# Optimization experiments

Measured on AMD Instinct MI355X. Metric: run time of the kernel, lower is better.

Reference implementation:

```python
import jax, jax.numpy as jnp
import numpy as np

BN_EPS = 1e-5


def setup_inputs() -> dict:
    key = jax.random.key(0)
    ks = jax.random.split(key, 6)
    B, N, M, C1, C2 = 8, 8192, 2048, 128, 256
    in_ch = C1 + C2  # 384
    return {
        "xyz1": jax.random.uniform(ks[0], (B, N, 3), dtype=jnp.float32),
        "xyz2": jax.random.uniform(ks[1], (B, M, 3), dtype=jnp.float32),
        "features1": jax.random.normal(ks[2], (B, C1, N), dtype=jnp.float32),
        "features2": jax.random.normal(ks[3], (B, C2, M), dtype=jnp.float32),
        # Conv1d(kernel_size=1, bias=False) weights, squeezed to [out, in]
        "conv_w0": jax.random.normal(ks[4], (256, in_ch), dtype=jnp.float32) * 0.05,
        "gamma0": jnp.ones((256,), dtype=jnp.float32),
        "beta0": jnp.zeros((256,), dtype=jnp.float32),
        "conv_w1": jax.random.normal(ks[5], (256, 256), dtype=jnp.float32) * 0.05,
        "gamma1": jnp.ones((256,), dtype=jnp.float32),
        "beta1": jnp.zeros((256,), dtype=jnp.float32),
    }


def _conv_bn_relu(x, w, gamma, beta):
    # 1x1 Conv1d (no bias) == per-point channel matmul: [B,Cin,N] -> [B,Cout,N]
    x = jnp.einsum("oc,bcn->bon", w, x)
    # BatchNorm1d in training mode: batch stats over (B, N), biased variance
    mu = jnp.mean(x, axis=(0, 2), keepdims=True)
    var = jnp.var(x, axis=(0, 2), keepdims=True)
    x = (x - mu) * jax.lax.rsqrt(var + BN_EPS)
    x = x * gamma[None, :, None] + beta[None, :, None]
    return jax.nn.relu(x)


def reference(xyz1, xyz2, features1, features2,
              conv_w0, gamma0, beta0, conv_w1, gamma1, beta1):
    # squared pairwise distances [B, N, M] (broadcast diff reduced over coord dim)
    diff = xyz1[:, :, None, :] - xyz2[:, None, :, :]  # [B,N,M,3]
    dists = jnp.sum(diff * diff, axis=-1)             # [B,N,M]
    idx = jnp.argmin(dists, axis=-1)                  # [B,N] nearest downsampled point

    # per-batch gather: features2[b, :, idx[b]] -> [B, C2, N]
    interp = jax.vmap(lambda f, i: f[:, i])(features2, idx)

    x = jnp.concatenate([features1, interp], axis=1)  # [B, C1+C2, N]
    x = _conv_bn_relu(x, conv_w0, gamma0, beta0)
    x = _conv_bn_relu(x, conv_w1, gamma1, beta1)
    return x
```

## Files before the change

### kernel.cpp

```cpp
#include <hip/hip_runtime.h>
#include <stdint.h>

typedef unsigned short u16;
typedef unsigned int u32;
typedef __attribute__((ext_vector_type(8))) short short8;
typedef __attribute__((ext_vector_type(4))) float floatx4;

__device__ __forceinline__ u16 f2b(float f) {
  union { float f; u32 u; } c; c.f = f;
  u32 u = c.u;
  u += 0x7fffu + ((u >> 16) & 1u);
  return (u16)(u >> 16);
}
__device__ __forceinline__ float b2f(u16 h) {
  union { u32 u; float f; } c; c.u = ((u32)h) << 16;
  return c.f;
}

__device__ __forceinline__ void glds16(const void* g, void* l) {
  __builtin_amdgcn_global_load_lds((__attribute__((address_space(1))) void*)g,
                                   (__attribute__((address_space(3))) void*)l, 16, 0, 0);
}

__global__ void prep_all_k(const float* __restrict__ xyz1, const float* __restrict__ xyz2,
                           float2* __restrict__ cand,
                           const float* __restrict__ f1, u16* __restrict__ f1t,
                           const float* __restrict__ f2, u16* __restrict__ f2t,
                           const float* __restrict__ w0, u16* __restrict__ w0b,
                           const float* __restrict__ w1, u16* __restrict__ w1b,
                           float* __restrict__ sums) {
  __shared__ __align__(16) char smem[9216];
  int blk = blockIdx.x, t = threadIdx.x;
  if (blk < 512) {
    float4* s2 = (float4*)smem;
    int nq = blk & 7, mq = (blk >> 3) & 7, b = blk >> 6;
    const float* x2 = xyz2 + ((size_t)b * 2048 + mq * 256) * 3;
    s2[t] = make_float4(x2[t * 3], x2[t * 3 + 1], x2[t * 3 + 2], 0.f);
    __syncthreads();
    int n0 = nq * 1024 + t;
    float px[4], py[4], pz[4];
#pragma unroll
    for (int q = 0; q < 4; q++) {
      const float* p1 = xyz1 + ((size_t)b * 8192 + n0 + q * 256) * 3;
      px[q] = p1[0]; py[q] = p1[1]; pz[q] = p1[2];
    }
    float best[4] = {3.0e38f, 3.0e38f, 3.0e38f, 3.0e38f};
    int bi[4] = {0, 0, 0, 0};
#pragma unroll 4
    for (int m = 0; m < 256; m++) {
      float4 qq = s2[m];
#pragma unroll
      for (int q = 0; q < 4; q++) {
        float dx = px[q] - qq.x, dy = py[q] - qq.y, dz = pz[q] - qq.z;
        float d = fmaf(dz, dz, fmaf(dy, dy, dx * dx));
        bool c = d < best[q];
        best[q] = c ? d : best[q];
        bi[q] = c ? m : bi[q];
      }
    }
#pragma unroll
    for (int q = 0; q < 4; q++) {
      int n = n0 + q * 256;
      cand[(size_t)mq * 65536 + (size_t)b * 8192 + n] =
          make_float2(best[q], __int_as_float(mq * 256 + bi[q]));
    }
  } else if (blk < 3584) {
    const float* in; u16* out; int C, N, bx, by, bz;
    if (blk < 2560) { int rel = blk - 512;  in = f1; out = f1t; C = 128; N = 8192; bx = rel & 127; by = (rel >> 7) & 1; bz = rel >> 8; }
    else            { int rel = blk - 2560; in = f2; out = f2t; C = 256; N = 2048; bx = rel & 31;  by = (rel >> 5) & 3; bz = rel >> 7; }
    u16 (*tile)[72] = (u16(*)[72])smem;
    int c0 = by * 64, n0 = bx * 64;
    const float* src = in + ((size_t)bz * C + c0) * N + n0;
#pragma unroll
    for (int i = 0; i < 4; i++) {
      int id = t + i * 256;
      int c = id >> 4, nq = (id & 15) * 4;
      float4 v = *(const float4*)(src + (size_t)c * N + nq);
      tile[nq + 0][c] = f2b(v.x);
      tile[nq + 1][c] = f2b(v.y);
      tile[nq + 2][c] = f2b(v.z);
      tile[nq + 3][c] = f2b(v.w);
    }
    __syncthreads();
    int n = t >> 2, ch = (t & 3) * 16;
    u16* dst = out + ((size_t)bz * N + n0 + n) * C + c0 + ch;
    *(uint4*)dst = *(const uint4*)&tile[n][ch];
    *(uint4*)(dst + 8) = *(const uint4*)&tile[n][ch + 8];
  } else {
    int rel = blk - 3584;
    int i = rel * 256 + t;
    if (rel < 384) w0b[i] = f2b(w0[i]);
    else { int j = i - 98304; w1b[j] = f2b(w1[j]); }
    if (rel < 4) sums[i] = 0.f;
  }
}

__global__ __launch_bounds__(512) void gemm1_k(const u16* __restrict__ w0b, const u16* __restrict__ f1t,
                                               const u16* __restrict__ f2t, const float2* __restrict__ cand,
                                               float* __restrict__ sum0, float* __restrict__ sq0,
                                               u16* __restrict__ y0) {
  __shared__ u16 As[256 * 64];
  __shared__ u16 Bs[128 * 64];
  __shared__ int sidx[128];
  int t = threadIdx.x;
  int pt0 = blockIdx.x * 128;
  int b = pt0 >> 13;
  if (t < 128) {
    int p = pt0 + t;
    float bd = 3.0e38f; int bi = 0;
#pragma unroll
    for (int qc = 0; qc < 8; qc++) {
      float2 c = cand[(size_t)qc * 65536 + p];
      if (c.x < bd) { bd = c.x; bi = __float_as_int(c.y); }
    }
    sidx[t] = bi;
  }
  floatx4 zero = {0.f, 0.f, 0.f, 0.f};
  floatx4 acc[4][4];
#pragma unroll
  for (int i = 0; i < 4; i++)
#pragma unroll
    for (int j = 0; j < 4; j++) acc[i][j] = zero;
  int lane = t & 63, wave = t >> 6;
  int wrow = (wave >> 1) * 64, wcol = (wave & 1) * 64;
  int lr = lane & 15, lq = lane >> 4;
  int srow = lane >> 3;
  int sch = ((lane & 7) ^ srow) * 8;
  __syncthreads();
  int prow[2], gidx[2];
#pragma unroll
  for (int i = 0; i < 2; i++) {
    prow[i] = (wave * 2 + i) * 8 + srow;
    gidx[i] = sidx[prow[i]];
  }

#pragma unroll
  for (int k0 = 0; k0 < 384; k0 += 64) {
    __syncthreads();
#pragma unroll
    for (int i = 0; i < 4; i++) {
      int chunkA = wave * 4 + i;
      glds16(w0b + (size_t)(chunkA * 8 + srow) * 384 + k0 + sch, &As[chunkA * 512]);
    }
    if (k0 < 128) {
#pragma unroll
      for (int i = 0; i < 2; i++)
        glds16(f1t + (size_t)(pt0 + prow[i]) * 128 + k0 + sch, &Bs[(wave * 2 + i) * 512]);
    } else {
#pragma unroll
      for (int i = 0; i < 2; i++)
        glds16(f2t + ((size_t)(b << 11) + gidx[i]) * 256 + (k0 - 128) + sch, &Bs[(wave * 2 + i) * 512]);
    }
    __syncthreads();
#pragma unroll
    for (int ks = 0; ks < 2; ks++) {
      short8 af[4], bf[4];
#pragma unroll
      for (int i = 0; i < 4; i++) {
        int row = wrow + i * 16 + lr;
        af[i] = *(const short8*)&As[row * 64 + ((((ks << 2) | lq) ^ (lr & 7)) << 3)];
      }
#pragma unroll
      for (int j = 0; j < 4; j++) {
        int row = wcol + j * 16 + lr;
        bf[j] = *(const short8*)&Bs[row * 64 + ((((ks << 2) | lq) ^ (lr & 7)) << 3)];
      }
#pragma unroll
      for (int i = 0; i < 4; i++)
#pragma unroll
        for (int j = 0; j < 4; j++)
          acc[i][j] = __builtin_amdgcn_mfma_f32_16x16x32_bf16(af[i], bf[j], acc[i][j], 0, 0, 0);
    }
  }
#pragma unroll
  for (int i = 0; i < 4; i++) {
#pragma unroll
    for (int j = 0; j < 4; j++) {
      int o = wrow + i * 16 + lq * 4;
      int p = pt0 + wcol + j * 16 + lr;
      uint2 pk;
      pk.x = (u32)f2b(acc[i][j][0]) | ((u32)f2b(acc[i][j][1]) << 16);
      pk.y = (u32)f2b(acc[i][j][2]) | ((u32)f2b(acc[i][j][3]) << 16);
      *(uint2*)&y0[(size_t)p * 256 + o] = pk;
    }
  }
  __syncthreads();
  float* red = (float*)As;
  red[t] = 0.f;
  __syncthreads();
#pragma unroll
  for (int i = 0; i < 4; i++) {
#pragma unroll
    for (int r = 0; r < 4; r++) {
      float s = acc[i][0][r] + acc[i][1][r] + acc[i][2][r] + acc[i][3][r];
      float q = acc[i][0][r] * acc[i][0][r] + acc[i][1][r] * acc[i][1][r] +
                acc[i][2][r] * acc[i][2][r] + acc[i][3][r] * acc[i][3][r];
#pragma unroll
      for (int m = 8; m >= 1; m >>= 1) { s += __shfl_xor(s, m); q += __shfl_xor(q, m); }
      if (lr == 0) {
        int o = wrow + i * 16 + lq * 4 + r;
        atomicAdd(&red[o], s);
        atomicAdd(&red[256 + o], q);
      }
    }
  }
  __syncthreads();
  if (t < 256) {
    atomicAdd(&sum0[t], red[t]);
    atomicAdd(&sq0[t], red[256 + t]);
  }
}

__global__ __launch_bounds__(512) void gemm2_k(const u16* __restrict__ w1b, const u16* __restrict__ y0,
                                               const float* __restrict__ sum0, const float* __restrict__ sq0,
                                               const float* __restrict__ gamma0, const float* __restrict__ beta0,
                                               float* __restrict__ sum1, float* __restrict__ sq1,
                                               u16* __restrict__ y1) {
  __shared__ u16 As[256 * 64];
  __shared__ u16 Bs[128 * 72];
  __shared__ float ssc[256], ssh[256];
  int t = threadIdx.x;
  if (t < 256) {
    float mean = sum0[t] * (1.f / 65536.f);
    float var = fmaxf(sq0[t] * (1.f / 65536.f) - mean * mean, 0.f);
    float r = rsqrtf(var + 1e-5f);
    float sc = gamma0[t] * r;
    ssc[t] = sc;
    ssh[t] = beta0[t] - mean * sc;
  }
  int pt0 = blockIdx.x * 128;
  floatx4 zero = {0.f, 0.f, 0.f, 0.f};
  floatx4 acc[4][4];
#pragma unroll
  for (int i = 0; i < 4; i++)
#pragma unroll
    for (int j = 0; j < 4; j++) acc[i][j] = zero;
  int lane = t & 63, wave = t >> 6;
  int wrow = (wave >> 1) * 64, wcol = (wave & 1) * 64;
  int lr = lane & 15, lq = lane >> 4;
  int srow = lane >> 3;
  int sch = ((lane & 7) ^ srow) * 8;

#pragma unroll
  for (int k0 = 0; k0 < 256; k0 += 64) {
    __syncthreads();
#pragma unroll
    for (int i = 0; i < 4; i++) {
      int chunkA = wave * 4 + i;
      glds16(w1b + (size_t)(chunkA * 8 + srow) * 256 + k0 + sch, &As[chunkA * 512]);
    }
#pragma unroll
    for (int i = 0; i < 2; i++) {
      int id = t + i * 512;
      int row = id >> 3, ch = (id & 7) * 8;
      uint4 raw = *(const uint4*)(y0 + (size_t)(pt0 + row) * 256 + k0 + ch);
      u32 rw[4] = {raw.x, raw.y, raw.z, raw.w};
      u32 ow[4];
#pragma unroll
      for (int w = 0; w < 4; w++) {
        int k = k0 + ch + w * 2;
        float v0 = b2f((u16)(rw[w] & 0xffffu));
        float v1 = b2f((u16)(rw[w] >> 16));
        v0 = fmaxf(v0 * ssc[k] + ssh[k], 0.f);
        v1 = fmaxf(v1 * ssc[k + 1] + ssh[k + 1], 0.f);
        ow[w] = (u32)f2b(v0) | ((u32)f2b(v1) << 16);
      }
      uint4 ov; ov.x = ow[0]; ov.y = ow[1]; ov.z = ow[2]; ov.w = ow[3];
      *(uint4*)&Bs[row * 72 + ch] = ov;
    }
    __syncthreads();
#pragma unroll
    for (int ks = 0; ks < 2; ks++) {
      int kk = ks * 32 + lq * 8;
      short8 af[4], bf[4];
#pragma unroll
      for (int i = 0; i < 4; i++) {
        int row = wrow + i * 16 + lr;
        af[i] = *(const short8*)&As[row * 64 + ((((ks << 2) | lq) ^ (lr & 7)) << 3)];
      }
#pragma unroll
      for (int j = 0; j < 4; j++) bf[j] = *(const short8*)&Bs[(wcol + j * 16 + lr) * 72 + kk];
#pragma unroll
      for (int i = 0; i < 4; i++)
#pragma unroll
        for (int j = 0; j < 4; j++)
          acc[i][j] = __builtin_amdgcn_mfma_f32_16x16x32_bf16(af[i], bf[j], acc[i][j], 0, 0, 0);
    }
  }
#pragma unroll
  for (int i = 0; i < 4; i++) {
#pragma unroll
    for (int j = 0; j < 4; j++) {
      int o = wrow + i * 16 + lq * 4;
      int p = pt0 + wcol + j * 16 + lr;
      uint2 pk;
      pk.x = (u32)f2b(acc[i][j][0]) | ((u32)f2b(acc[i][j][1]) << 16);
      pk.y = (u32)f2b(acc[i][j][2]) | ((u32)f2b(acc[i][j][3]) << 16);
      *(uint2*)&y1[(size_t)p * 256 + o] = pk;
    }
  }
  __syncthreads();
  float* red = (float*)As;
  red[t] = 0.f;
  __syncthreads();
#pragma unroll
  for (int i = 0; i < 4; i++) {
#pragma unroll
    for (int r = 0; r < 4; r++) {
      float s = acc[i][0][r] + acc[i][1][r] + acc[i][2][r] + acc[i][3][r];
      float q = acc[i][0][r] * acc[i][0][r] + acc[i][1][r] * acc[i][1][r] +
                acc[i][2][r] * acc[i][2][r] + acc[i][3][r] * acc[i][3][r];
#pragma unroll
      for (int m = 8; m >= 1; m >>= 1) { s += __shfl_xor(s, m); q += __shfl_xor(q, m); }
      if (lr == 0) {
        int o = wrow + i * 16 + lq * 4 + r;
        atomicAdd(&red[o], s);
        atomicAdd(&red[256 + o], q);
      }
    }
  }
  __syncthreads();
  if (t < 256) {
    atomicAdd(&sum1[t], red[t]);
    atomicAdd(&sq1[t], red[256 + t]);
  }
}

__global__ void finalize_k(const u16* __restrict__ y1, const float* __restrict__ sum1,
                           const float* __restrict__ sq1, const float* __restrict__ gamma1,
                           const float* __restrict__ beta1, float* __restrict__ out) {
  __shared__ float tile[64][65];
  __shared__ float fs[64], fh[64];
  int b = blockIdx.z, o0 = blockIdx.y * 64, n0 = blockIdx.x * 64;
  int t = threadIdx.x;
  if (t < 64) {
    int o = o0 + t;
    float mean = sum1[o] * (1.f / 65536.f);
    float var = fmaxf(sq1[o] * (1.f / 65536.f) - mean * mean, 0.f);
    float r = rsqrtf(var + 1e-5f);
    float sc = gamma1[o] * r;
    fs[t] = sc;
    fh[t] = beta1[o] - mean * sc;
  }
  __syncthreads();
  int pl = t >> 2, ch = (t & 3) * 16;
  const u16* src = y1 + ((size_t)(b * 8192 + n0 + pl)) * 256 + o0 + ch;
  uint4 r0 = *(const uint4*)src;
  uint4 r1 = *(const uint4*)(src + 8);
  u16 hv[16];
  *(uint4*)&hv[0] = r0;
  *(uint4*)&hv[8] = r1;
#pragma unroll
  for (int e = 0; e < 16; e++) {
    float v = b2f(hv[e]) * fs[ch + e] + fh[ch + e];
    tile[pl][ch + e] = fmaxf(v, 0.f);
  }
  __syncthreads();
  int ol = t >> 2, nch = (t & 3) * 16;
  float* dst = out + ((size_t)(b * 256 + o0 + ol)) * 8192 + n0 + nch;
#pragma unroll
  for (int j = 0; j < 16; j += 4) {
    float4 v = make_float4(tile[nch + j][ol], tile[nch + j + 1][ol],
                           tile[nch + j + 2][ol], tile[nch + j + 3][ol]);
    *(float4*)(dst + j) = v;
  }
}

extern "C" void kernel_launch(void* const* d_in, const int* in_sizes, int n_in,
                              void* d_out, int out_size, void* d_ws, size_t ws_size,
                              hipStream_t stream) {
  const float* xyz1      = (const float*)d_in[0];
  const float* xyz2      = (const float*)d_in[1];
  const float* features1 = (const float*)d_in[2];
  const float* features2 = (const float*)d_in[3];
  const float* conv_w0   = (const float*)d_in[4];
  const float* gamma0    = (const float*)d_in[5];
  const float* beta0     = (const float*)d_in[6];
  const float* conv_w1   = (const float*)d_in[7];
  const float* gamma1    = (const float*)d_in[8];
  const float* beta1     = (const float*)d_in[9];
  float* out = (float*)d_out;

  char* ws = (char*)d_ws;
  size_t off = 0;
  auto alloc = [&](size_t bytes) {
    char* p = ws + off;
    off = (off + bytes + 4095) & ~(size_t)4095;
    return p;
  };
  float*  sums = (float*)alloc(4 * 256 * 4);
  u16*    w0b  = (u16*)alloc(256 * 384 * 2);
  u16*    w1b  = (u16*)alloc(256 * 256 * 2);
  float2* cand = (float2*)alloc((size_t)8 * 65536 * 8);
  u16*    f1t  = (u16*)alloc((size_t)65536 * 128 * 2);
  u16*    f2t  = (u16*)alloc((size_t)16384 * 256 * 2);
  u16*    y0   = (u16*)alloc((size_t)65536 * 256 * 2);
  u16*    y1   = (u16*)alloc((size_t)65536 * 256 * 2);

  prep_all_k<<<dim3(4224), 256, 0, stream>>>(xyz1, xyz2, cand, features1, f1t,
                                             features2, f2t, conv_w0, w0b, conv_w1, w1b, sums);
  gemm1_k<<<dim3(512), 512, 0, stream>>>(w0b, f1t, f2t, cand, sums + 0, sums + 256, y0);
  gemm2_k<<<dim3(512), 512, 0, stream>>>(w1b, y0, sums + 0, sums + 256, gamma0, beta0,
                                         sums + 512, sums + 768, y1);
  finalize_k<<<dim3(128, 4, 8), 256, 0, stream>>>(y1, sums + 512, sums + 768, gamma1, beta1, out);
}
```

Baseline: 243.3 us.

## Split GEMM output channels across grid y with 256-thread blocks

Both GEMM kernels now tile output channels into two 128-wide halves along blockIdx.y and use 256-thread blocks instead of 512, doubling the grid to 1024 blocks. The goal is more blocks per CU and better occupancy and load balance across the 256 CUs, since smaller LDS and thread footprints let four blocks co-reside. The cost is that each activation tile (including the gathered features2 rows and the BN+ReLU transform in gemm2) is loaded and recomputed twice, and twice as many atomic stat updates occur.

```diff
diff --git a/kernel.cpp b/kernel.cpp
--- a/kernel.cpp
+++ b/kernel.cpp
@@ -95,15 +95,16 @@
   }
 }
 
-__global__ __launch_bounds__(512) void gemm1_k(const u16* __restrict__ w0b, const u16* __restrict__ f1t,
-                                               const u16* __restrict__ f2t, const float2* __restrict__ cand,
-                                               float* __restrict__ sum0, float* __restrict__ sq0,
-                                               u16* __restrict__ y0) {
-  __shared__ u16 As[256 * 64];
+__global__ __launch_bounds__(256, 4) void gemm1_k(const u16* __restrict__ w0b, const u16* __restrict__ f1t,
+                                                  const u16* __restrict__ f2t, const float2* __restrict__ cand,
+                                                  float* __restrict__ sum0, float* __restrict__ sq0,
+                                                  u16* __restrict__ y0) {
+  __shared__ u16 As[128 * 64];
   __shared__ u16 Bs[128 * 64];
   __shared__ int sidx[128];
   int t = threadIdx.x;
   int pt0 = blockIdx.x * 128;
+  int o0 = blockIdx.y * 128;
   int b = pt0 >> 13;
   if (t < 128) {
     int p = pt0 + t;
@@ -127,10 +128,10 @@
   int srow = lane >> 3;
   int sch = ((lane & 7) ^ srow) * 8;
   __syncthreads();
-  int prow[2], gidx[2];
-#pragma unroll
-  for (int i = 0; i < 2; i++) {
-    prow[i] = (wave * 2 + i) * 8 + srow;
+  int prow[4], gidx[4];
+#pragma unroll
+  for (int i = 0; i < 4; i++) {
+    prow[i] = (wave * 4 + i) * 8 + srow;
     gidx[i] = sidx[prow[i]];
   }
 
@@ -140,16 +141,16 @@
 #pragma unroll
     for (int i = 0; i < 4; i++) {
       int chunkA = wave * 4 + i;
-      glds16(w0b + (size_t)(chunkA * 8 + srow) * 384 + k0 + sch, &As[chunkA * 512]);
+      glds16(w0b + (size_t)(o0 + chunkA * 8 + srow) * 384 + k0 + sch, &As[chunkA * 512]);
     }
     if (k0 < 128) {
 #pragma unroll
-      for (int i = 0; i < 2; i++)
-        glds16(f1t + (size_t)(pt0 + prow[i]) * 128 + k0 + sch, &Bs[(wave * 2 + i) * 512]);
+      for (int i = 0; i < 4; i++)
+        glds16(f1t + (size_t)(pt0 + prow[i]) * 128 + k0 + sch, &Bs[(wave * 4 + i) * 512]);
     } else {
 #pragma unroll
-      for (int i = 0; i < 2; i++)
-        glds16(f2t + ((size_t)(b << 11) + gidx[i]) * 256 + (k0 - 128) + sch, &Bs[(wave * 2 + i) * 512]);
+      for (int i = 0; i < 4; i++)
+        glds16(f2t + ((size_t)(b << 11) + gidx[i]) * 256 + (k0 - 128) + sch, &Bs[(wave * 4 + i) * 512]);
     }
     __syncthreads();
 #pragma unroll
@@ -176,7 +177,7 @@
   for (int i = 0; i < 4; i++) {
 #pragma unroll
     for (int j = 0; j < 4; j++) {
-      int o = wrow + i * 16 + lq * 4;
+      int o = o0 + wrow + i * 16 + lq * 4;
       int p = pt0 + wcol + j * 16 + lr;
       uint2 pk;
       pk.x = (u32)f2b(acc[i][j][0]) | ((u32)f2b(acc[i][j][1]) << 16);
@@ -186,7 +187,7 @@
   }
   __syncthreads();
   float* red = (float*)As;
-  red[t] = 0.f;
+  red[t] = 0.f; red[t + 256] = 0.f;
   __syncthreads();
 #pragma unroll
   for (int i = 0; i < 4; i++) {
@@ -205,22 +206,22 @@
     }
   }
   __syncthreads();
-  if (t < 256) {
-    atomicAdd(&sum0[t], red[t]);
-    atomicAdd(&sq0[t], red[256 + t]);
-  }
-}
-
-__global__ __launch_bounds__(512) void gemm2_k(const u16* __restrict__ w1b, const u16* __restrict__ y0,
-                                               const float* __restrict__ sum0, const float* __restrict__ sq0,
-                                               const float* __restrict__ gamma0, const float* __restrict__ beta0,
-                                               float* __restrict__ sum1, float* __restrict__ sq1,
-                                               u16* __restrict__ y1) {
-  __shared__ u16 As[256 * 64];
+  if (t < 128) {
+    atomicAdd(&sum0[o0 + t], red[t]);
+    atomicAdd(&sq0[o0 + t], red[256 + t]);
+  }
+}
+
+__global__ __launch_bounds__(256, 4) void gemm2_k(const u16* __restrict__ w1b, const u16* __restrict__ y0,
+                                                  const float* __restrict__ sum0, const float* __restrict__ sq0,
+                                                  const float* __restrict__ gamma0, const float* __restrict__ beta0,
+                                                  float* __restrict__ sum1, float* __restrict__ sq1,
+                                                  u16* __restrict__ y1) {
+  __shared__ u16 As[128 * 64];
   __shared__ u16 Bs[128 * 72];
   __shared__ float ssc[256], ssh[256];
   int t = threadIdx.x;
-  if (t < 256) {
+  {
     float mean = sum0[t] * (1.f / 65536.f);
     float var = fmaxf(sq0[t] * (1.f / 65536.f) - mean * mean, 0.f);
     float r = rsqrtf(var + 1e-5f);
@@ -229,6 +230,7 @@
     ssh[t] = beta0[t] - mean * sc;
   }
   int pt0 = blockIdx.x * 128;
+  int o0 = blockIdx.y * 128;
   floatx4 zero = {0.f, 0.f, 0.f, 0.f};
   floatx4 acc[4][4];
 #pragma unroll
@@ -247,11 +249,11 @@
 #pragma unroll
     for (int i = 0; i < 4; i++) {
       int chunkA = wave * 4 + i;
-      glds16(w1b + (size_t)(chunkA * 8 + srow) * 256 + k0 + sch, &As[chunkA * 512]);
-    }
-#pragma unroll
-    for (int i = 0; i < 2; i++) {
-      int id = t + i * 512;
+      glds16(w1b + (size_t)(o0 + chunkA * 8 + srow) * 256 + k0 + sch, &As[chunkA * 512]);
+    }
+#pragma unroll
+    for (int i = 0; i < 4; i++) {
+      int id = t + i * 256;
       int row = id >> 3, ch = (id & 7) * 8;
       uint4 raw = *(const uint4*)(y0 + (size_t)(pt0 + row) * 256 + k0 + ch);
       u32 rw[4] = {raw.x, raw.y, raw.z, raw.w};
@@ -291,7 +293,7 @@
   for (int i = 0; i < 4; i++) {
 #pragma unroll
     for (int j = 0; j < 4; j++) {
-      int o = wrow + i * 16 + lq * 4;
+      int o = o0 + wrow + i * 16 + lq * 4;
       int p = pt0 + wcol + j * 16 + lr;
       uint2 pk;
       pk.x = (u32)f2b(acc[i][j][0]) | ((u32)f2b(acc[i][j][1]) << 16);
@@ -301,7 +303,7 @@
   }
   __syncthreads();
   float* red = (float*)As;
-  red[t] = 0.f;
+  red[t] = 0.f; red[t + 256] = 0.f;
   __syncthreads();
 #pragma unroll
   for (int i = 0; i < 4; i++) {
@@ -320,9 +322,9 @@
     }
   }
   __syncthreads();
-  if (t < 256) {
-    atomicAdd(&sum1[t], red[t]);
-    atomicAdd(&sq1[t], red[256 + t]);
+  if (t < 128) {
+    atomicAdd(&sum1[o0 + t], red[t]);
+    atomicAdd(&sq1[o0 + t], red[256 + t]);
   }
 }
 
@@ -399,8 +401,8 @@
 
   prep_all_k<<<dim3(4224), 256, 0, stream>>>(xyz1, xyz2, cand, features1, f1t,
                                              features2, f2t, conv_w0, w0b, conv_w1, w1b, sums);
-  gemm1_k<<<dim3(512), 512, 0, stream>>>(w0b, f1t, f2t, cand, sums + 0, sums + 256, y0);
-  gemm2_k<<<dim3(512), 512, 0, stream>>>(w1b, y0, sums + 0, sums + 256, gamma0, beta0,
-                                         sums + 512, sums + 768, y1);
+  gemm1_k<<<dim3(512, 2), 256, 0, stream>>>(w0b, f1t, f2t, cand, sums + 0, sums + 256, y0);
+  gemm2_k<<<dim3(512, 2), 256, 0, stream>>>(w1b, y0, sums + 0, sums + 256, gamma0, beta0,
+                                            sums + 512, sums + 768, y1);
   finalize_k<<<dim3(128, 4, 8), 256, 0, stream>>>(y1, sums + 512, sums + 768, gamma1, beta1, out);
 }
```

Result: slower. 252.8 us (+3.9%).

## Stage full-K point tile in LDS and read weights directly from global

Applied to the files above, without the earlier changes.

Both GEMM kernels now use 64-point tiles with 256 threads. Each block loads its whole K slice of activations (the gathered f1/f2 rows, or the normalized y0) into padded LDS once. The weight fragments are read straight from global memory, which should mostly hit in cache, so the per-K-step global_load_lds staging and the barriers around it go away. The trade-off is that each wave pulls its weight rows from global or L2 on every k-step with no LDS reuse. It also doubles the block count and uses larger LDS tiles, which changes occupancy.

```diff
diff --git a/kernel.cpp b/kernel.cpp
--- a/kernel.cpp
+++ b/kernel.cpp
@@ -15,11 +15,6 @@
 __device__ __forceinline__ float b2f(u16 h) {
   union { u32 u; float f; } c; c.u = ((u32)h) << 16;
   return c.f;
-}
-
-__device__ __forceinline__ void glds16(const void* g, void* l) {
-  __builtin_amdgcn_global_load_lds((__attribute__((address_space(1))) void*)g,
-                                   (__attribute__((address_space(3))) void*)l, 16, 0, 0);
 }
 
 __global__ void prep_all_k(const float* __restrict__ xyz1, const float* __restrict__ xyz2,
@@ -95,17 +90,16 @@
   }
 }
 
-__global__ __launch_bounds__(512) void gemm1_k(const u16* __restrict__ w0b, const u16* __restrict__ f1t,
-                                               const u16* __restrict__ f2t, const float2* __restrict__ cand,
-                                               float* __restrict__ sum0, float* __restrict__ sq0,
-                                               u16* __restrict__ y0) {
-  __shared__ u16 As[256 * 64];
-  __shared__ u16 Bs[128 * 64];
-  __shared__ int sidx[128];
+__global__ __launch_bounds__(256, 3) void gemm1_k(const u16* __restrict__ w0b, const u16* __restrict__ f1t,
+                                                  const u16* __restrict__ f2t, const float2* __restrict__ cand,
+                                                  float* __restrict__ sum0, float* __restrict__ sq0,
+                                                  u16* __restrict__ y0) {
+  __shared__ __align__(16) u16 Bs[64 * 392];
+  __shared__ int sidx[64];
   int t = threadIdx.x;
-  int pt0 = blockIdx.x * 128;
+  int pt0 = blockIdx.x * 64;
   int b = pt0 >> 13;
-  if (t < 128) {
+  if (t < 64) {
     int p = pt0 + t;
     float bd = 3.0e38f; int bi = 0;
 #pragma unroll
@@ -115,69 +109,54 @@
     }
     sidx[t] = bi;
   }
+  __syncthreads();
+#pragma unroll
+  for (int i = 0; i < 4; i++) {
+    int id = i * 256 + t;
+    int p = id >> 4, kc = (id & 15) * 8;
+    uint4 v = *(const uint4*)(f1t + (size_t)(pt0 + p) * 128 + kc);
+    *(uint4*)&Bs[p * 392 + kc] = v;
+  }
+#pragma unroll
+  for (int i = 0; i < 8; i++) {
+    int id = i * 256 + t;
+    int p = id >> 5, kc = (id & 31) * 8;
+    uint4 v = *(const uint4*)(f2t + ((size_t)(b << 11) + sidx[p]) * 256 + kc);
+    *(uint4*)&Bs[p * 392 + 128 + kc] = v;
+  }
+  __syncthreads();
+
+  int lane = t & 63, wave = t >> 6;
+  int wrow = wave * 64;
+  int lr = lane & 15, lq = lane >> 4;
+  const u16* ab = w0b + (size_t)(wrow + lr) * 384 + lq * 8;
+  const u16* bb = &Bs[lr * 392 + lq * 8];
   floatx4 zero = {0.f, 0.f, 0.f, 0.f};
   floatx4 acc[4][4];
 #pragma unroll
   for (int i = 0; i < 4; i++)
 #pragma unroll
     for (int j = 0; j < 4; j++) acc[i][j] = zero;
-  int lane = t & 63, wave = t >> 6;
-  int wrow = (wave >> 1) * 64, wcol = (wave & 1) * 64;
-  int lr = lane & 15, lq = lane >> 4;
-  int srow = lane >> 3;
-  int sch = ((lane & 7) ^ srow) * 8;
-  __syncthreads();
-  int prow[2], gidx[2];
-#pragma unroll
-  for (int i = 0; i < 2; i++) {
-    prow[i] = (wave * 2 + i) * 8 + srow;
-    gidx[i] = sidx[prow[i]];
-  }
-
-#pragma unroll
-  for (int k0 = 0; k0 < 384; k0 += 64) {
-    __syncthreads();
-#pragma unroll
-    for (int i = 0; i < 4; i++) {
-      int chunkA = wave * 4 + i;
-      glds16(w0b + (size_t)(chunkA * 8 + srow) * 384 + k0 + sch, &As[chunkA * 512]);
-    }
-    if (k0 < 128) {
-#pragma unroll
-      for (int i = 0; i < 2; i++)
-        glds16(f1t + (size_t)(pt0 + prow[i]) * 128 + k0 + sch, &Bs[(wave * 2 + i) * 512]);
-    } else {
-#pragma unroll
-      for (int i = 0; i < 2; i++)
-        glds16(f2t + ((size_t)(b << 11) + gidx[i]) * 256 + (k0 - 128) + sch, &Bs[(wave * 2 + i) * 512]);
-    }
-    __syncthreads();
-#pragma unroll
-    for (int ks = 0; ks < 2; ks++) {
-      short8 af[4], bf[4];
-#pragma unroll
-      for (int i = 0; i < 4; i++) {
-        int row = wrow + i * 16 + lr;
-        af[i] = *(const short8*)&As[row * 64 + ((((ks << 2) | lq) ^ (lr & 7)) << 3)];
-      }
-#pragma unroll
-      for (int j = 0; j < 4; j++) {
-        int row = wcol + j * 16 + lr;
-        bf[j] = *(const short8*)&Bs[row * 64 + ((((ks << 2) | lq) ^ (lr & 7)) << 3)];
-      }
-#pragma unroll
-      for (int i = 0; i < 4; i++)
-#pragma unroll
-        for (int j = 0; j < 4; j++)
-          acc[i][j] = __builtin_amdgcn_mfma_f32_16x16x32_bf16(af[i], bf[j], acc[i][j], 0, 0, 0);
-    }
+
+#pragma unroll
+  for (int k0 = 0; k0 < 384; k0 += 32) {
+    short8 af[4], bf[4];
+#pragma unroll
+    for (int i = 0; i < 4; i++) af[i] = *(const short8*)(ab + (size_t)i * 16 * 384 + k0);
+#pragma unroll
+    for (int j = 0; j < 4; j++) bf[j] = *(const short8*)(bb + j * 16 * 392 + k0);
+#pragma unroll
+    for (int i = 0; i < 4; i++)
+#pragma unroll
+      for (int j = 0; j < 4; j++)
+        acc[i][j] = __builtin_amdgcn_mfma_f32_16x16x32_bf16(af[i], bf[j], acc[i][j], 0, 0, 0);
   }
 #pragma unroll
   for (int i = 0; i < 4; i++) {
 #pragma unroll
     for (int j = 0; j < 4; j++) {
       int o = wrow + i * 16 + lq * 4;
-      int p = pt0 + wcol + j * 16 + lr;
+      int p = pt0 + j * 16 + lr;
       uint2 pk;
       pk.x = (u32)f2b(acc[i][j][0]) | ((u32)f2b(acc[i][j][1]) << 16);
       pk.y = (u32)f2b(acc[i][j][2]) | ((u32)f2b(acc[i][j][3]) << 16);
@@ -185,8 +164,8 @@
     }
   }
   __syncthreads();
-  float* red = (float*)As;
-  red[t] = 0.f;
+  float* red = (float*)Bs;
+  red[t] = 0.f; red[t + 256] = 0.f;
   __syncthreads();
 #pragma unroll
   for (int i = 0; i < 4; i++) {
@@ -205,22 +184,19 @@
     }
   }
   __syncthreads();
-  if (t < 256) {
-    atomicAdd(&sum0[t], red[t]);
-    atomicAdd(&sq0[t], red[256 + t]);
-  }
-}
-
-__global__ __launch_bounds__(512) void gemm2_k(const u16* __restrict__ w1b, const u16* __restrict__ y0,
-                                               const float* __restrict__ sum0, const float* __restrict__ sq0,
-                                               const float* __restrict__ gamma0, const float* __restrict__ beta0,
-                                               float* __restrict__ sum1, float* __restrict__ sq1,
-                                               u16* __restrict__ y1) {
-  __shared__ u16 As[256 * 64];
-  __shared__ u16 Bs[128 * 72];
+  atomicAdd(&sum0[t], red[t]);
+  atomicAdd(&sq0[t], red[256 + t]);
+}
+
+__global__ __launch_bounds__(256, 3) void gemm2_k(const u16* __restrict__ w1b, const u16* __restrict__ y0,
+                                                  const float* __restrict__ sum0, const float* __restrict__ sq0,
+                                                  const float* __restrict__ gamma0, const float* __restrict__ beta0,
+                                                  float* __restrict__ sum1, float* __restrict__ sq1,
+                                                  u16* __restrict__ y1) {
+  __shared__ __align__(16) u16 Bs[64 * 264];
   __shared__ float ssc[256], ssh[256];
   int t = threadIdx.x;
-  if (t < 256) {
+  {
     float mean = sum0[t] * (1.f / 65536.f);
     float var = fmaxf(sq0[t] * (1.f / 65536.f) - mean * mean, 0.f);
     float r = rsqrtf(var + 1e-5f);
@@ -228,71 +204,61 @@
     ssc[t] = sc;
     ssh[t] = beta0[t] - mean * sc;
   }
-  int pt0 = blockIdx.x * 128;
+  int pt0 = blockIdx.x * 64;
+  __syncthreads();
+#pragma unroll
+  for (int i = 0; i < 8; i++) {
+    int id = i * 256 + t;
+    int p = id >> 5, kc = (id & 31) * 8;
+    uint4 raw = *(const uint4*)(y0 + (size_t)(pt0 + p) * 256 + kc);
+    float4 sc0 = *(const float4*)&ssc[kc], sc1 = *(const float4*)&ssc[kc + 4];
+    float4 sh0 = *(const float4*)&ssh[kc], sh1 = *(const float4*)&ssh[kc + 4];
+    u32 rw[4] = {raw.x, raw.y, raw.z, raw.w};
+    float scs[8] = {sc0.x, sc0.y, sc0.z, sc0.w, sc1.x, sc1.y, sc1.z, sc1.w};
+    float shs[8] = {sh0.x, sh0.y, sh0.z, sh0.w, sh1.x, sh1.y, sh1.z, sh1.w};
+    u32 ow[4];
+#pragma unroll
+    for (int w = 0; w < 4; w++) {
+      float v0 = fmaxf(b2f((u16)(rw[w] & 0xffffu)) * scs[w * 2] + shs[w * 2], 0.f);
+      float v1 = fmaxf(b2f((u16)(rw[w] >> 16)) * scs[w * 2 + 1] + shs[w * 2 + 1], 0.f);
+      ow[w] = (u32)f2b(v0) | ((u32)f2b(v1) << 16);
+    }
+    uint4 ov; ov.x = ow[0]; ov.y = ow[1]; ov.z = ow[2]; ov.w = ow[3];
+    *(uint4*)&Bs[p * 264 + kc] = ov;
+  }
+  __syncthreads();
+
+  int lane = t & 63, wave = t >> 6;
+  int wrow = wave * 64;
+  int lr = lane & 15, lq = lane >> 4;
+  const u16* ab = w1b + (size_t)(wrow + lr) * 256 + lq * 8;
+  const u16* bb = &Bs[lr * 264 + lq * 8];
   floatx4 zero = {0.f, 0.f, 0.f, 0.f};
   floatx4 acc[4][4];
 #pragma unroll
   for (int i = 0; i < 4; i++)
 #pragma unroll
     for (int j = 0; j < 4; j++) acc[i][j] = zero;
-  int lane = t & 63, wave = t >> 6;
-  int wrow = (wave >> 1) * 64, wcol = (wave & 1) * 64;
-  int lr = lane & 15, lq = lane >> 4;
-  int srow = lane >> 3;
-  int sch = ((lane & 7) ^ srow) * 8;
-
-#pragma unroll
-  for (int k0 = 0; k0 < 256; k0 += 64) {
-    __syncthreads();
-#pragma unroll
-    for (int i = 0; i < 4; i++) {
-      int chunkA = wave * 4 + i;
-      glds16(w1b + (size_t)(chunkA * 8 + srow) * 256 + k0 + sch, &As[chunkA * 512]);
-    }
-#pragma unroll
-    for (int i = 0; i < 2; i++) {
-      int id = t + i * 512;
-      int row = id >> 3, ch = (id & 7) * 8;
-      uint4 raw = *(const uint4*)(y0 + (size_t)(pt0 + row) * 256 + k0 + ch);
-      u32 rw[4] = {raw.x, raw.y, raw.z, raw.w};
-      u32 ow[4];
-#pragma unroll
-      for (int w = 0; w < 4; w++) {
-        int k = k0 + ch + w * 2;
-        float v0 = b2f((u16)(rw[w] & 0xffffu));
-        float v1 = b2f((u16)(rw[w] >> 16));
-        v0 = fmaxf(v0 * ssc[k] + ssh[k], 0.f);
-        v1 = fmaxf(v1 * ssc[k + 1] + ssh[k + 1], 0.f);
-        ow[w] = (u32)f2b(v0) | ((u32)f2b(v1) << 16);
-      }
-      uint4 ov; ov.x = ow[0]; ov.y = ow[1]; ov.z = ow[2]; ov.w = ow[3];
-      *(uint4*)&Bs[row * 72 + ch] = ov;
-    }
-    __syncthreads();
-#pragma unroll
-    for (int ks = 0; ks < 2; ks++) {
-      int kk = ks * 32 + lq * 8;
-      short8 af[4], bf[4];
-#pragma unroll
-      for (int i = 0; i < 4; i++) {
-        int row = wrow + i * 16 + lr;
-        af[i] = *(const short8*)&As[row * 64 + ((((ks << 2) | lq) ^ (lr & 7)) << 3)];
-      }
-#pragma unroll
-      for (int j = 0; j < 4; j++) bf[j] = *(const short8*)&Bs[(wcol + j * 16 + lr) * 72 + kk];
-#pragma unroll
-      for (int i = 0; i < 4; i++)
-#pragma unroll
-        for (int j = 0; j < 4; j++)
-          acc[i][j] = __builtin_amdgcn_mfma_f32_16x16x32_bf16(af[i], bf[j], acc[i][j], 0, 0, 0);
-    }
+
+#pragma unroll
+  for (int k0 = 0; k0 < 256; k0 += 32) {
+    short8 af[4], bf[4];
+#pragma unroll
+    for (int i = 0; i < 4; i++) af[i] = *(const short8*)(ab + (size_t)i * 16 * 256 + k0);
+#pragma unroll
+    for (int j = 0; j < 4; j++) bf[j] = *(const short8*)(bb + j * 16 * 264 + k0);
+#pragma unroll
+    for (int i = 0; i < 4; i++)
+#pragma unroll
+      for (int j = 0; j < 4; j++)
+        acc[i][j] = __builtin_amdgcn_mfma_f32_16x16x32_bf16(af[i], bf[j], acc[i][j], 0, 0, 0);
   }
 #pragma unroll
   for (int i = 0; i < 4; i++) {
 #pragma unroll
     for (int j = 0; j < 4; j++) {
       int o = wrow + i * 16 + lq * 4;
-      int p = pt0 + wcol + j * 16 + lr;
+      int p = pt0 + j * 16 + lr;
       uint2 pk;
       pk.x = (u32)f2b(acc[i][j][0]) | ((u32)f2b(acc[i][j][1]) << 16);
       pk.y = (u32)f2b(acc[i][j][2]) | ((u32)f2b(acc[i][j][3]) << 16);
@@ -300,8 +266,8 @@
     }
   }
   __syncthreads();
-  float* red = (float*)As;
-  red[t] = 0.f;
+  float* red = (float*)Bs;
+  red[t] = 0.f; red[t + 256] = 0.f;
   __syncthreads();
 #pragma unroll
   for (int i = 0; i < 4; i++) {
@@ -320,10 +286,8 @@
     }
   }
   __syncthreads();
-  if (t < 256) {
-    atomicAdd(&sum1[t], red[t]);
-    atomicAdd(&sq1[t], red[256 + t]);
-  }
+  atomicAdd(&sum1[t], red[t]);
+  atomicAdd(&sq1[t], red[256 + t]);
 }
 
 __global__ void finalize_k(const u16* __restrict__ y1, const float* __restrict__ sum1,
@@ -399,8 +363,8 @@
 
   prep_all_k<<<dim3(4224), 256, 0, stream>>>(xyz1, xyz2, cand, features1, f1t,
                                              features2, f2t, conv_w0, w0b, conv_w1, w1b, sums);
-  gemm1_k<<<dim3(512), 512, 0, stream>>>(w0b, f1t, f2t, cand, sums + 0, sums + 256, y0);
-  gemm2_k<<<dim3(512), 512, 0, stream>>>(w1b, y0, sums + 0, sums + 256, gamma0, beta0,
-                                         sums + 512, sums + 768, y1);
+  gemm1_k<<<dim3(1024), 256, 0, stream>>>(w0b, f1t, f2t, cand, sums + 0, sums + 256, y0);
+  gemm2_k<<<dim3(1024), 256, 0, stream>>>(w1b, y0, sums + 0, sums + 256, gamma0, beta0,
+                                          sums + 512, sums + 768, y1);
   finalize_k<<<dim3(128, 4, 8), 256, 0, stream>>>(y1, sums + 512, sums + 768, gamma1, beta1, out);
 }
```

New measurement: 273.2 us. +12.3%, slower.
